# Optimization experiments

Measured on AMD Instinct MI355X. Metric: run time of the kernel, lower is better.

The kernel has to match this reference:

```python
import jax, jax.numpy as jnp
import numpy as np

B, Q, K, C, H, DH, OUT = 32, 512, 512, 256, 8, 32, 256


def setup_inputs() -> dict:
    key = jax.random.key(0)
    ks = jax.random.split(key, 11)
    s = 1.0 / np.sqrt(C)
    return {
        "q_data": jax.random.normal(ks[0], (B, Q, C), jnp.float32),
        "m_data": jax.random.normal(ks[1], (B, K, C), jnp.float32),
        "bias": jax.random.normal(ks[2], (B, 1, Q, K), jnp.float32),
        "nonbatched_bias": jax.random.normal(ks[3], (H, Q, K), jnp.float32),
        "query_w": jax.random.normal(ks[4], (C, H, DH), jnp.float32) * s,
        "key_w": jax.random.normal(ks[5], (C, H, DH), jnp.float32) * s,
        "value_w": jax.random.normal(ks[6], (C, H, DH), jnp.float32) * s,
        "gating_w": jax.random.normal(ks[7], (C, H, DH), jnp.float32) * s,
        "gating_b": jax.random.normal(ks[8], (H, DH), jnp.float32),
        "output_w": jax.random.normal(ks[9], (H, DH, OUT), jnp.float32) * (1.0 / np.sqrt(H * DH)),
        "output_b": jax.random.normal(ks[10], (OUT,), jnp.float32),
    }


def reference(q_data, m_data, bias, nonbatched_bias, query_w, key_w, value_w,
              gating_w, gating_b, output_w, output_b):
    key_dim = query_w.shape[-1]  # per-head key dim
    q = jnp.einsum('bqa,ahc->bqhc', q_data, query_w) * key_dim ** (-0.5)
    k = jnp.einsum('bka,ahc->bkhc', m_data, key_w)
    v = jnp.einsum('bka,ahc->bkhc', m_data, value_w)
    logits = jnp.einsum('bqhc,bkhc->bhqk', q, k) + bias  # [B,H,Q,K]
    logits = logits + nonbatched_bias[None]  # broadcast over batch
    logits = jnp.clip(logits, -1e8, 1e8)
    weights = jax.nn.softmax(logits, axis=-1)
    weighted_avg = jnp.einsum('bhqk,bkhc->bqhc', weights, v)
    gate = jax.nn.sigmoid(jnp.einsum('bqc,chv->bqhv', q_data, gating_w) + gating_b)
    weighted_avg = weighted_avg * gate
    return jnp.einsum('bqhc,hco->bqo', weighted_avg, output_w) + output_b
```

## Files before the change

kernel.cpp:

```cpp
#include <hip/hip_runtime.h>

typedef unsigned short u16;
typedef __attribute__((ext_vector_type(4))) short short4v;
typedef __attribute__((ext_vector_type(8))) short bf16x8;
typedef __attribute__((ext_vector_type(4))) float f32x4;

union Pack8 { u16 h[8]; int4 v; bf16x8 b; };
union Frag8 { bf16x8 v8; short4v h4[2]; };

__device__ __forceinline__ f32x4 mfma16(bf16x8 a, bf16x8 b, f32x4 c) {
    return __builtin_amdgcn_mfma_f32_16x16x32_bf16(a, b, c, 0, 0, 0);
}

__device__ __forceinline__ float bf2f(u16 u) {
    unsigned int x = ((unsigned int)u) << 16;
    return __builtin_bit_cast(float, x);
}

__device__ __forceinline__ u16 f2bf(float f) {
    unsigned int u = __builtin_bit_cast(unsigned int, f);
    u += 0x7FFF + ((u >> 16) & 1);
    return (u16)(u >> 16);
}

__global__ __launch_bounds__(256) void prep_w2(
    const float* __restrict__ qw, const float* __restrict__ kw,
    const float* __restrict__ vw, const float* __restrict__ gw,
    const float* __restrict__ ow,
    u16* __restrict__ wtq, u16* __restrict__ wtm, u16* __restrict__ wto)
{
    const int which = blockIdx.z;
    const float* s = which == 0 ? qw : which == 1 ? kw : which == 2 ? vw
                   : which == 3 ? gw : ow;
    u16* d; int roff;
    if (which == 0)      { d = wtq; roff = 0; }
    else if (which == 3) { d = wtq; roff = 256; }
    else if (which == 1) { d = wtm; roff = 0; }
    else if (which == 2) { d = wtm; roff = 256; }
    else                 { d = wto; roff = 0; }

    const int n0 = blockIdx.x * 64;
    const int c0 = blockIdx.y * 64;

    __shared__ float T[64][68];
    const int rr = threadIdx.x >> 2;
    const int sg = threadIdx.x & 3;
    #pragma unroll
    for (int j = 0; j < 4; ++j) {
        float4 v = *(const float4*)(&s[(size_t)(c0 + rr) * 256 + n0 + sg * 16 + j * 4]);
        *(float4*)(&T[rr][sg * 16 + j * 4]) = v;
    }
    __syncthreads();
    #pragma unroll
    for (int j = 0; j < 4; ++j) {
        union { u16 h[4]; uint2 v; } p;
        #pragma unroll
        for (int e = 0; e < 4; ++e)
            p.h[e] = f2bf(T[sg * 16 + j * 4 + e][rr]);
        *(uint2*)(&d[(size_t)(roff + n0 + rr) * 256 + c0 + sg * 16 + j * 4]) = p.v;
    }
}

__global__ __launch_bounds__(256) void proj128(
    const float* __restrict__ q_data, const float* __restrict__ m_data,
    const u16* __restrict__ wtq, const u16* __restrict__ wtm,
    const float* __restrict__ gating_b,
    u16* __restrict__ qbuf, u16* __restrict__ kbuf,
    u16* __restrict__ vbuf, u16* __restrict__ gbuf)
{
    const int src = blockIdx.z;
    const float* X = src ? m_data : q_data;
    const u16* W = src ? wtm : wtq;

    const int m0 = blockIdx.x * 128;
    const int n0 = blockIdx.y * 128;

    __shared__ __align__(16) u16 SMEM[2][128][72];
    #define Xs (SMEM[0])
    #define Ws (SMEM[1])

    const int tid  = threadIdx.x;
    const int wave = tid >> 6;
    const int wm   = wave >> 1, wn = wave & 1;
    const int lane = tid & 63;
    const int l16  = lane & 15;
    const int quad = lane >> 4;

    const f32x4 kZero = {0.f, 0.f, 0.f, 0.f};
    f32x4 acc[4][4];
    #pragma unroll
    for (int i = 0; i < 4; ++i)
        #pragma unroll
        for (int j = 0; j < 4; ++j) acc[i][j] = kZero;

    const int r  = tid >> 1;
    const int cs = (tid & 1) * 32;

    for (int k0 = 0; k0 < 256; k0 += 64) {
        __syncthreads();
        #pragma unroll
        for (int i = 0; i < 4; ++i) {
            const float4* xp = (const float4*)(&X[(size_t)(m0 + r) * 256 + k0 + cs + i * 8]);
            float4 xa = xp[0], xb = xp[1];
            Pack8 pk;
            pk.h[0] = f2bf(xa.x); pk.h[1] = f2bf(xa.y);
            pk.h[2] = f2bf(xa.z); pk.h[3] = f2bf(xa.w);
            pk.h[4] = f2bf(xb.x); pk.h[5] = f2bf(xb.y);
            pk.h[6] = f2bf(xb.z); pk.h[7] = f2bf(xb.w);
            *(int4*)(&Xs[r][cs + i * 8]) = pk.v;
            *(int4*)(&Ws[r][cs + i * 8]) = *(const int4*)(&W[(size_t)(n0 + r) * 256 + k0 + cs + i * 8]);
        }
        __syncthreads();
        #pragma unroll
        for (int ks = 0; ks < 2; ++ks) {
            bf16x8 a[4], bb[4];
            #pragma unroll
            for (int mf = 0; mf < 4; ++mf)
                a[mf] = *(const bf16x8*)(&Xs[wm * 64 + mf * 16 + l16][ks * 32 + quad * 8]);
            #pragma unroll
            for (int nf = 0; nf < 4; ++nf)
                bb[nf] = *(const bf16x8*)(&Ws[wn * 64 + nf * 16 + l16][ks * 32 + quad * 8]);
            #pragma unroll
            for (int mf = 0; mf < 4; ++mf)
                #pragma unroll
                for (int nf = 0; nf < 4; ++nf)
                    acc[mf][nf] = mfma16(a[mf], bb[nf], acc[mf][nf]);
        }
    }

    const bool second = (n0 >= 256);
    const int b = m0 >> 9, qi0 = m0 & 511;

    if (src == 1 && second) {
        __syncthreads();
        u16* T = &SMEM[0][0][0];
        #pragma unroll
        for (int nf = 0; nf < 4; ++nf) {
            const int nl_ = wn * 64 + nf * 16 + l16;
            #pragma unroll
            for (int mf = 0; mf < 4; ++mf)
                #pragma unroll
                for (int rr = 0; rr < 4; ++rr) {
                    const int ml = wm * 64 + mf * 16 + quad * 4 + rr;
                    T[nl_ * 136 + ml] = f2bf(acc[mf][nf][rr]);
                }
        }
        __syncthreads();
        const int row = tid >> 1, half = tid & 1;
        const int nl = (n0 - 256) + row;
        const int h = nl >> 5, c = nl & 31;
        u16* dst = &vbuf[((size_t)(b * 8 + h) * 32 + c) * 512 + qi0 + half * 64];
        #pragma unroll
        for (int i = 0; i < 8; ++i)
            *(int4*)(&dst[i * 8]) = *(const int4*)(&T[row * 136 + half * 64 + i * 8]);
        return;
    }

    #pragma unroll
    for (int nf = 0; nf < 4; ++nf) {
        const int ng = n0 + wn * 64 + nf * 16 + l16;
        const int nl = second ? (ng - 256) : ng;
        const int h = nl >> 5, c = nl & 31;
        #pragma unroll
        for (int mf = 0; mf < 4; ++mf) {
            #pragma unroll
            for (int rr = 0; rr < 4; ++rr) {
                const int m = m0 + wm * 64 + mf * 16 + quad * 4 + rr;
                const int qi = m & 511;
                float v = acc[mf][nf][rr];
                size_t hidx = (((size_t)(b * 8 + h) * 512 + qi) * 32 + c);
                if (src == 0) {
                    if (!second) {
                        qbuf[hidx] = f2bf(v * 0.17677669529663689f);
                    } else {
                        float g = 1.0f / (1.0f + __expf(-(v + gating_b[nl])));
                        gbuf[(size_t)m * 256 + nl] = f2bf(g);
                    }
                } else {
                    kbuf[hidx] = f2bf(v);
                }
            }
        }
    }
    #undef Xs
    #undef Ws
}

__global__ __launch_bounds__(256) void attn_kernel(
    const u16* __restrict__ qbuf, const u16* __restrict__ kbuf,
    const u16* __restrict__ vbuf, const float* __restrict__ bias,
    const float* __restrict__ nb, const u16* __restrict__ gbuf,
    u16* __restrict__ waG)
{
    const int b = blockIdx.z, h = blockIdx.y, q0 = blockIdx.x * 64;
    const int tid  = threadIdx.x;
    const int wave = tid >> 6;
    const int lane = tid & 63;
    const int l16  = lane & 15;
    const int quad = lane >> 4;

    __shared__ __align__(16) u16 Ks[64][40];
    __shared__ __align__(16) u16 Vs[32][72];
    __shared__ __align__(16) u16 Os[4][16][40];

    const int qrow_base = q0 + wave * 16;
    bf16x8 aQ = *(const bf16x8*)(&qbuf[((b * 8 + h) * 512 + qrow_base + l16) * 32 + quad * 8]);

    const f32x4 kZero = {0.f, 0.f, 0.f, 0.f};
    f32x4 oacc[2] = {kZero, kZero};
    float lsum = 0.f;

    const int krow = tid >> 2, kseg = tid & 3;
    const int vr = tid >> 3,  vseg = tid & 7;
    const u16* kbase = &kbuf[(size_t)(b * 8 + h) * 512 * 32];
    const u16* vbase = &vbuf[(size_t)(b * 8 + h) * 32 * 512];
    const float* blp = &bias[((size_t)b * 512 + qrow_base + l16) * 512];
    const float* nlp = &nb[((size_t)h * 512 + qrow_base + l16) * 512];

    for (int kt = 0; kt < 8; ++kt) {
        const int kk0 = kt * 64;
        float4 bb[4], nn[4];
        #pragma unroll
        for (int kn = 0; kn < 4; ++kn) {
            bb[kn] = *(const float4*)(&blp[kk0 + kn * 16 + quad * 4]);
            nn[kn] = *(const float4*)(&nlp[kk0 + kn * 16 + quad * 4]);
        }
        __syncthreads();
        *(int4*)(&Ks[krow][kseg * 8]) = *(const int4*)(&kbase[(kk0 + krow) * 32 + kseg * 8]);
        *(int4*)(&Vs[vr][vseg * 8])   = *(const int4*)(&vbase[vr * 512 + kk0 + vseg * 8]);
        __syncthreads();

        float p[4][4];
        #pragma unroll
        for (int kn = 0; kn < 4; ++kn) {
            f32x4 cb = {bb[kn].x + nn[kn].x, bb[kn].y + nn[kn].y,
                        bb[kn].z + nn[kn].z, bb[kn].w + nn[kn].w};
            bf16x8 aK = *(const bf16x8*)(&Ks[kn * 16 + l16][quad * 8]);
            f32x4 st = mfma16(aK, aQ, cb);
            #pragma unroll
            for (int rr = 0; rr < 4; ++rr) {
                float pv = __expf(st[rr]);
                p[kn][rr] = pv;
                lsum += pv;
            }
        }

        #pragma unroll
        for (int pr = 0; pr < 2; ++pr) {
            Frag8 bP;
            #pragma unroll
            for (int rr = 0; rr < 4; ++rr) {
                bP.h4[0][rr] = (short)f2bf(p[2 * pr][rr]);
                bP.h4[1][rr] = (short)f2bf(p[2 * pr + 1][rr]);
            }
            #pragma unroll
            for (int ct = 0; ct < 2; ++ct) {
                Frag8 aV;
                aV.h4[0] = *(const short4v*)(&Vs[ct * 16 + l16][pr * 32 + quad * 4]);
                aV.h4[1] = *(const short4v*)(&Vs[ct * 16 + l16][pr * 32 + 16 + quad * 4]);
                oacc[ct] = mfma16(aV.v8, bP.v8, oacc[ct]);
            }
        }
    }

    lsum += __shfl_xor(lsum, 16, 64);
    lsum += __shfl_xor(lsum, 32, 64);
    const float linv = 1.0f / lsum;

    #pragma unroll
    for (int ct = 0; ct < 2; ++ct)
        #pragma unroll
        for (int rr = 0; rr < 4; ++rr)
            Os[wave][l16][ct * 16 + quad * 4 + rr] = f2bf(oacc[ct][rr] * linv);

    __asm__ __volatile__("" ::: "memory");

    const int orow = lane >> 2, osg = lane & 3;
    Pack8 ov, gv;
    ov.v = *(const int4*)(&Os[wave][orow][osg * 8]);
    size_t gidx = ((size_t)(b * 512 + q0 + wave * 16 + orow)) * 256 + h * 32 + osg * 8;
    gv.v = *(const int4*)(&gbuf[gidx]);
    Pack8 outv;
    #pragma unroll
    for (int i = 0; i < 8; ++i)
        outv.h[i] = f2bf(bf2f(ov.h[i]) * bf2f(gv.h[i]));
    *(int4*)(&waG[gidx]) = outv.v;
}

__global__ __launch_bounds__(256) void out_gemm128(
    const u16* __restrict__ waG, const u16* __restrict__ wto,
    const float* __restrict__ out_b, float* __restrict__ out)
{
    const int m0 = blockIdx.x * 128;
    const int n0 = blockIdx.y * 128;

    __shared__ __align__(16) u16 Xs[128][72];
    __shared__ __align__(16) u16 Ws[128][72];

    const int tid  = threadIdx.x;
    const int wave = tid >> 6;
    const int wm   = wave >> 1, wn = wave & 1;
    const int lane = tid & 63;
    const int l16  = lane & 15;
    const int quad = lane >> 4;

    const f32x4 kZero = {0.f, 0.f, 0.f, 0.f};
    f32x4 acc[4][4];
    #pragma unroll
    for (int i = 0; i < 4; ++i)
        #pragma unroll
        for (int j = 0; j < 4; ++j) acc[i][j] = kZero;

    const int r  = tid >> 1;
    const int cs = (tid & 1) * 32;

    for (int k0 = 0; k0 < 256; k0 += 64) {
        __syncthreads();
        #pragma unroll
        for (int i = 0; i < 4; ++i) {
            *(int4*)(&Xs[r][cs + i * 8]) = *(const int4*)(&waG[(size_t)(m0 + r) * 256 + k0 + cs + i * 8]);
            *(int4*)(&Ws[r][cs + i * 8]) = *(const int4*)(&wto[(size_t)(n0 + r) * 256 + k0 + cs + i * 8]);
        }
        __syncthreads();
        #pragma unroll
        for (int ks = 0; ks < 2; ++ks) {
            bf16x8 a[4], bb[4];
            #pragma unroll
            for (int mf = 0; mf < 4; ++mf)
                a[mf] = *(const bf16x8*)(&Xs[wm * 64 + mf * 16 + l16][ks * 32 + quad * 8]);
            #pragma unroll
            for (int nf = 0; nf < 4; ++nf)
                bb[nf] = *(const bf16x8*)(&Ws[wn * 64 + nf * 16 + l16][ks * 32 + quad * 8]);
            #pragma unroll
            for (int mf = 0; mf < 4; ++mf)
                #pragma unroll
                for (int nf = 0; nf < 4; ++nf)
                    acc[mf][nf] = mfma16(a[mf], bb[nf], acc[mf][nf]);
        }
    }

    #pragma unroll
    for (int nf = 0; nf < 4; ++nf) {
        const int n = n0 + wn * 64 + nf * 16 + l16;
        const float ob = out_b[n];
        #pragma unroll
        for (int mf = 0; mf < 4; ++mf) {
            #pragma unroll
            for (int rr = 0; rr < 4; ++rr) {
                const int m = m0 + wm * 64 + mf * 16 + quad * 4 + rr;
                out[(size_t)m * 256 + n] = acc[mf][nf][rr] + ob;
            }
        }
    }
}

extern "C" void kernel_launch(void* const* d_in, const int* in_sizes, int n_in,
                              void* d_out, int out_size, void* d_ws, size_t ws_size,
                              hipStream_t stream)
{
    const float* q_data = (const float*)d_in[0];
    const float* m_data = (const float*)d_in[1];
    const float* bias   = (const float*)d_in[2];
    const float* nb     = (const float*)d_in[3];
    const float* qw     = (const float*)d_in[4];
    const float* kw     = (const float*)d_in[5];
    const float* vw     = (const float*)d_in[6];
    const float* gw     = (const float*)d_in[7];
    const float* gb     = (const float*)d_in[8];
    const float* ow     = (const float*)d_in[9];
    const float* ob     = (const float*)d_in[10];

    char* ws = (char*)d_ws;
    u16* wtq  = (u16*)ws;
    u16* wtm  = wtq + 131072;
    u16* wto  = wtm + 131072;
    u16* qbuf = wto + 65536;
    u16* kbuf = qbuf + 4194304;
    u16* vbuf = kbuf + 4194304;
    u16* gbuf = vbuf + 4194304;
    u16* waG  = gbuf + 4194304;

    prep_w2<<<dim3(4, 4, 5), 256, 0, stream>>>(qw, kw, vw, gw, ow, wtq, wtm, wto);
    proj128<<<dim3(128, 4, 2), 256, 0, stream>>>(q_data, m_data, wtq, wtm, gb,
                                                 qbuf, kbuf, vbuf, gbuf);
    attn_kernel<<<dim3(8, 8, 32), 256, 0, stream>>>(qbuf, kbuf, vbuf, bias, nb,
                                                    gbuf, waG);
    out_gemm128<<<dim3(128, 2), 256, 0, stream>>>(waG, wto, ob, (float*)d_out);
}
```

Measured before the change: 242.5 us.

## Stage projection outputs and bias tiles through shared memory for coalesced access

The projection kernel now writes every output tile (q, k, gate) into shared memory first, then stores it to global memory with contiguous 16-byte vectors instead of scattered 2-byte stores. The attention kernel loads the bias and nonbatched-bias tile cooperatively, with each thread reading contiguous row segments, adds the two into a shared-memory float tile, and each wave then reads its MFMA accumulator seed from there. This targets the poorly coalesced global stores and bias loads. In exchange it adds extra barriers and shared-memory traffic, the attention kernel's LDS use grows by about 17 KB, and the bias loads are no longer issued ahead of the first barrier.

```diff
diff --git a/kernel.cpp b/kernel.cpp
--- a/kernel.cpp
+++ b/kernel.cpp
@@ -131,9 +131,10 @@
     const bool second = (n0 >= 256);
     const int b = m0 >> 9, qi0 = m0 & 511;
 
+    __syncthreads();
+    u16* T = &SMEM[0][0][0];
+
     if (src == 1 && second) {
-        __syncthreads();
-        u16* T = &SMEM[0][0][0];
         #pragma unroll
         for (int nf = 0; nf < 4; ++nf) {
             const int nl_ = wn * 64 + nf * 16 + l16;
@@ -158,28 +159,44 @@
 
     #pragma unroll
     for (int nf = 0; nf < 4; ++nf) {
-        const int ng = n0 + wn * 64 + nf * 16 + l16;
-        const int nl = second ? (ng - 256) : ng;
-        const int h = nl >> 5, c = nl & 31;
+        const int nl_ = wn * 64 + nf * 16 + l16;
+        const int ng = n0 + nl_;
         #pragma unroll
         for (int mf = 0; mf < 4; ++mf) {
             #pragma unroll
             for (int rr = 0; rr < 4; ++rr) {
-                const int m = m0 + wm * 64 + mf * 16 + quad * 4 + rr;
-                const int qi = m & 511;
+                const int ml = wm * 64 + mf * 16 + quad * 4 + rr;
                 float v = acc[mf][nf][rr];
-                size_t hidx = (((size_t)(b * 8 + h) * 512 + qi) * 32 + c);
-                if (src == 0) {
-                    if (!second) {
-                        qbuf[hidx] = f2bf(v * 0.17677669529663689f);
-                    } else {
-                        float g = 1.0f / (1.0f + __expf(-(v + gating_b[nl])));
-                        gbuf[(size_t)m * 256 + nl] = f2bf(g);
-                    }
+                u16 val;
+                if (src == 0 && !second) {
+                    val = f2bf(v * 0.17677669529663689f);
+                } else if (src == 0) {
+                    val = f2bf(1.0f / (1.0f + __expf(-(v + gating_b[ng - 256]))));
                 } else {
-                    kbuf[hidx] = f2bf(v);
+                    val = f2bf(v);
                 }
+                T[ml * 136 + nl_] = val;
             }
+        }
+    }
+    __syncthreads();
+
+    if (src == 0 && second) {
+        const int ml = tid >> 1, sub = tid & 1;
+        u16* dst = &gbuf[(size_t)(m0 + ml) * 256 + (n0 - 256) + sub * 64];
+        #pragma unroll
+        for (int i = 0; i < 8; ++i)
+            *(int4*)(&dst[i * 8]) = *(const int4*)(&T[ml * 136 + sub * 64 + i * 8]);
+    } else {
+        u16* D = (src == 0) ? qbuf : kbuf;
+        const int hl = tid & 3, h0 = n0 >> 5;
+        #pragma unroll
+        for (int p = 0; p < 2; ++p) {
+            const int ml = p * 64 + (tid >> 2);
+            u16* dst = &D[((size_t)(b * 8 + h0 + hl) * 512 + qi0 + ml) * 32];
+            #pragma unroll
+            for (int i = 0; i < 4; ++i)
+                *(int4*)(&dst[i * 8]) = *(const int4*)(&T[ml * 136 + hl * 32 + i * 8]);
         }
     }
     #undef Xs
@@ -199,9 +216,10 @@
     const int l16  = lane & 15;
     const int quad = lane >> 4;
 
-    __shared__ __align__(16) u16 Ks[64][40];
-    __shared__ __align__(16) u16 Vs[32][72];
-    __shared__ __align__(16) u16 Os[4][16][40];
+    __shared__ __align__(16) u16  Ks[64][40];
+    __shared__ __align__(16) u16  Vs[32][72];
+    __shared__ __align__(16) float Bs[64][68];
+    __shared__ __align__(16) u16  Os[4][16][40];
 
     const int qrow_base = q0 + wave * 16;
     bf16x8 aQ = *(const bf16x8*)(&qbuf[((b * 8 + h) * 512 + qrow_base + l16) * 32 + quad * 8]);
@@ -212,29 +230,31 @@
 
     const int krow = tid >> 2, kseg = tid & 3;
     const int vr = tid >> 3,  vseg = tid & 7;
+    const int bq = tid >> 2,  bsg = tid & 3;
     const u16* kbase = &kbuf[(size_t)(b * 8 + h) * 512 * 32];
     const u16* vbase = &vbuf[(size_t)(b * 8 + h) * 32 * 512];
-    const float* blp = &bias[((size_t)b * 512 + qrow_base + l16) * 512];
-    const float* nlp = &nb[((size_t)h * 512 + qrow_base + l16) * 512];
+    const float* biasb = &bias[((size_t)b * 512 + q0) * 512];
+    const float* nbb   = &nb[((size_t)h * 512 + q0) * 512];
 
     for (int kt = 0; kt < 8; ++kt) {
         const int kk0 = kt * 64;
-        float4 bb[4], nn[4];
-        #pragma unroll
-        for (int kn = 0; kn < 4; ++kn) {
-            bb[kn] = *(const float4*)(&blp[kk0 + kn * 16 + quad * 4]);
-            nn[kn] = *(const float4*)(&nlp[kk0 + kn * 16 + quad * 4]);
-        }
         __syncthreads();
         *(int4*)(&Ks[krow][kseg * 8]) = *(const int4*)(&kbase[(kk0 + krow) * 32 + kseg * 8]);
         *(int4*)(&Vs[vr][vseg * 8])   = *(const int4*)(&vbase[vr * 512 + kk0 + vseg * 8]);
+        #pragma unroll
+        for (int i = 0; i < 4; ++i) {
+            const int c = bsg * 16 + i * 4;
+            float4 bv = *(const float4*)(&biasb[(size_t)bq * 512 + kk0 + c]);
+            float4 nv = *(const float4*)(&nbb[(size_t)bq * 512 + kk0 + c]);
+            float4 s = make_float4(bv.x + nv.x, bv.y + nv.y, bv.z + nv.z, bv.w + nv.w);
+            *(float4*)(&Bs[bq][c]) = s;
+        }
         __syncthreads();
 
         float p[4][4];
         #pragma unroll
         for (int kn = 0; kn < 4; ++kn) {
-            f32x4 cb = {bb[kn].x + nn[kn].x, bb[kn].y + nn[kn].y,
-                        bb[kn].z + nn[kn].z, bb[kn].w + nn[kn].w};
+            f32x4 cb = *(const f32x4*)(&Bs[wave * 16 + l16][kn * 16 + quad * 4]);
             bf16x8 aK = *(const bf16x8*)(&Ks[kn * 16 + l16][quad * 8]);
             f32x4 st = mfma16(aK, aQ, cb);
             #pragma unroll
```

Result: faster. 224.7 us (-7.4%).
